# Kernel optimization log

Measured on AMD Instinct MI355X. Metric: run time of the kernel, lower is better.

## Reference

```python
import jax, jax.numpy as jnp
import numpy as np

B, CIN, COUT, K, H, W = 8, 256, 256, 4, 128, 128
BN_EPS = 1e-5


def setup_inputs() -> dict:
    key = jax.random.key(0)
    ks = jax.random.split(key, 12)
    n = lambda i, shape, scale: jax.random.normal(ks[i], shape, jnp.float32) * scale
    return {
        "x": jax.random.normal(ks[0], (B, CIN, H, W), jnp.float32),
        "conv_w": n(1, (COUT, CIN), 0.05),
        "conv_b": n(2, (COUT,), 0.02),
        "off_w": n(3, (K, 2, CIN), 0.02),   # k offset convs, each 1x1 -> 2 channels
        "off_b": n(4, (K, 2), 0.02),
        "wgt_w": n(5, (K, CIN), 0.05),      # weight conv 1x1 -> k channels (softmax over k)
        "wgt_b": n(6, (K,), 0.02),
        "gamma": 1.0 + n(7, (COUT,), 0.1),
        "beta": n(8, (COUT,), 0.1),
        "run_mean": n(9, (COUT,), 0.05),
        "run_var": 1.0 + 0.1 * jax.random.uniform(ks[10], (COUT,), jnp.float32),
        "out_w": n(11, (CIN, COUT), 0.05),
        "out_b": jnp.zeros((CIN,), jnp.float32),
    }


def bilinear_sample(img, gx, gy):
    """F.grid_sample(mode='bilinear', padding_mode='zeros', align_corners=True).
    img: [B,C,H,W]; gx,gy: [B,H,W] normalized coords in [-1,1]."""
    b, c, h, w = img.shape
    x = (gx + 1.0) * 0.5 * (w - 1)  # unnormalize (align_corners=True)
    y = (gy + 1.0) * 0.5 * (h - 1)
    x0 = jnp.floor(x)
    y0 = jnp.floor(y)
    wx1 = x - x0
    wy1 = y - y0
    imgf = img.reshape(b, c, h * w)

    def gather(xi, yi, wgt):
        valid = (xi >= 0) & (xi <= w - 1) & (yi >= 0) & (yi <= h - 1)
        xic = jnp.clip(xi, 0, w - 1).astype(jnp.int32)
        yic = jnp.clip(yi, 0, h - 1).astype(jnp.int32)
        idx = (yic * w + xic).reshape(b, 1, h * w)
        v = jnp.take_along_axis(imgf, idx, axis=2).reshape(b, c, h, w)
        return v * (wgt * valid)[:, None]  # zeros padding: OOB corners contribute 0

    return (gather(x0, y0, (1 - wx1) * (1 - wy1))
            + gather(x0 + 1, y0, wx1 * (1 - wy1))
            + gather(x0, y0 + 1, (1 - wx1) * wy1)
            + gather(x0 + 1, y0 + 1, wx1 * wy1))


def reference(x, conv_w, conv_b, off_w, off_b, wgt_w, wgt_b,
              gamma, beta, run_mean, run_var, out_w, out_b):
    # 1x1 projection conv
    proj = jnp.einsum('bchw,oc->bohw', x, conv_w) + conv_b[:, None, None]
    # k offset branches at once: [K,B,2,H,W]
    flows = jnp.einsum('bchw,koc->kbohw', x, off_w) + off_b[:, None, :, None, None]
    # per-branch softmax weights: [B,K,H,W]
    logits = jnp.einsum('bchw,kc->bkhw', x, wgt_w) + wgt_b[None, :, None, None]
    weights = jax.nn.softmax(logits, axis=1)
    # base grid + flow, normalized to [-1,1]
    grid_x = jnp.arange(W, dtype=jnp.float32)[None, None, None, :]  # broadcast over k,b,h
    grid_y = jnp.arange(H, dtype=jnp.float32)[None, None, :, None]
    vx = grid_x + flows[:, :, 0]  # [K,B,H,W]
    vy = grid_y + flows[:, :, 1]
    gxn = 2.0 * vx / max(W - 1, 1) - 1.0
    gyn = 2.0 * vy / max(H - 1, 1) - 1.0
    feats = jax.vmap(lambda gx, gy: bilinear_sample(proj, gx, gy))(gxn, gyn)  # [K,B,C,H,W]
    # repeat_interleave(weights, out_ch) * cat(feats) then split+sum == weighted sum over k
    fsum = jnp.einsum('kbchw,bkhw->bchw', feats, weights)
    feat = proj + fsum  # dropout in eval mode = identity
    # BatchNorm2d (eval: running stats)
    inv = gamma / jnp.sqrt(run_var + BN_EPS)
    feat = (feat - run_mean[:, None, None]) * inv[:, None, None] + beta[:, None, None]
    return jnp.einsum('bchw,oc->bohw', feat, out_w) + out_b[:, None, None]
```

## Files before the change

kernel.cpp:

```cpp
#include <hip/hip_runtime.h>
#include <cstddef>
#include <cstdint>

#define B_    8
#define CIN_  256
#define COUT_ 256
#define K_    4
#define H_    128
#define W_    128
#define HW_   (H_ * W_)
#define P_    (B_ * HW_)
#define BN_EPS 1e-5f

typedef __attribute__((ext_vector_type(8))) short bf16x8_t;
typedef __attribute__((ext_vector_type(4))) float f32x4_t;

__device__ __forceinline__ unsigned short f2bf(float f) {
    unsigned int u = __float_as_uint(f);
    u += 0x7fffu + ((u >> 16) & 1u);
    return (unsigned short)(u >> 16);
}
__device__ __forceinline__ float2 up2(unsigned int u) {
    return make_float2(__uint_as_float(u << 16), __uint_as_float(u & 0xffff0000u));
}
__device__ __forceinline__ void fma2(float2& d, float s, float2 v) {
    d.x = fmaf(s, v.x, d.x);
    d.y = fmaf(s, v.y, d.y);
}

#define GL2LDS(g, l)                                                                     \
    __builtin_amdgcn_global_load_lds((const __attribute__((address_space(1))) void*)(g), \
                                     (__attribute__((address_space(3))) void*)(l), 16, 0, 0)

__global__ __launch_bounds__(256) void k_prep(
    const float* __restrict__ conv_w, const float* __restrict__ out_w,
    const float* __restrict__ gamma, const float* __restrict__ beta,
    const float* __restrict__ rmean, const float* __restrict__ rvar,
    const float* __restrict__ out_b, const float* __restrict__ off_w,
    const float* __restrict__ wgt_w,
    unsigned short* __restrict__ wA, unsigned short* __restrict__ wB,
    float* __restrict__ bias2, unsigned short* __restrict__ wB2)
{
    const int t = threadIdx.x;
    if (blockIdx.x < 64) {
        const int i = (blockIdx.x * 256 + t) * 4;
        float4 a = *(const float4*)&conv_w[i];
        uint2 pa;
        pa.x = (unsigned)f2bf(a.x) | ((unsigned)f2bf(a.y) << 16);
        pa.y = (unsigned)f2bf(a.z) | ((unsigned)f2bf(a.w) << 16);
        *(uint2*)&wA[i] = pa;
    } else if (blockIdx.x == 64) {
        __shared__ float sinv[256], sd[256];
        const float iv = gamma[t] * rsqrtf(rvar[t] + BN_EPS);
        sinv[t] = iv;
        sd[t]   = beta[t] - rmean[t] * iv;
        __syncthreads();
        float acc = out_b[t];
        for (int c = 0; c < 256; c += 4) {
            const float4 wv = *(const float4*)&out_w[t * 256 + c];
            acc += sd[c] * wv.x + sd[c + 1] * wv.y + sd[c + 2] * wv.z + sd[c + 3] * wv.w;
            uint2 p;
            p.x = (unsigned)f2bf(wv.x * sinv[c])     | ((unsigned)f2bf(wv.y * sinv[c + 1]) << 16);
            p.y = (unsigned)f2bf(wv.z * sinv[c + 2]) | ((unsigned)f2bf(wv.w * sinv[c + 3]) << 16);
            *(uint2*)&wB[t * 256 + c] = p;
        }
        bias2[t] = acc;
    } else {
        for (int j = 0; j < 16; ++j) {
            float v = 0.f;
            if (j < 8)       v = off_w[j * 256 + t];
            else if (j < 12) v = wgt_w[(j - 8) * 256 + t];
            wB2[j * 256 + t] = f2bf(v);
        }
    }
}

__global__ __launch_bounds__(512, 2) void k_fproj(
    const float* __restrict__ x, const unsigned short* __restrict__ wA,
    const unsigned short* __restrict__ wB2, const float* __restrict__ conv_b,
    const float* __restrict__ off_b, const float* __restrict__ wgt_b,
    unsigned short* __restrict__ proj, float4* __restrict__ tabW,
    int4* __restrict__ tabI)
{
    __shared__ alignas(16) char smem[57856];
    char*           AsB  = smem;
    char*           Bs   = smem + 16384;
    float*          fbuf = (float*)(smem + 49152);
    unsigned short* ep   = (unsigned short*)smem;

    const int t   = threadIdx.x;
    const int w   = t >> 6;
    const int l   = t & 63;
    const int lr  = l & 15;
    const int lq  = l >> 4;
    const int wm2 = w & 1;
    const int wn4 = w >> 1;
    const int chg = t & 15;
    const int pxg = t >> 4;
    const int p0  = blockIdx.x * 128;
    const float* xb = x + (size_t)(p0 >> 14) * (256 * HW_) + (p0 & (HW_ - 1)) + pxg * 4;

    f32x4_t acc[4][4];
#pragma unroll
    for (int i = 0; i < 4; ++i)
#pragma unroll
        for (int j = 0; j < 4; ++j) acc[i][j] = (f32x4_t){0.f, 0.f, 0.f, 0.f};
    f32x4_t acc2 = (f32x4_t){0.f, 0.f, 0.f, 0.f};

    float4 f[4], fn[4];
#pragma unroll
    for (int i = 0; i < 4; ++i)
        f[i] = *(const float4*)&xb[(size_t)(chg * 4 + i) * HW_];

    for (int ks = 0; ks < 4; ++ks) {
#pragma unroll
        for (int o = 0; o < 4; ++o) {
            const int px = pxg * 4 + o;
            const float v0 = (o == 0) ? f[0].x : (o == 1) ? f[0].y : (o == 2) ? f[0].z : f[0].w;
            const float v1 = (o == 0) ? f[1].x : (o == 1) ? f[1].y : (o == 2) ? f[1].z : f[1].w;
            const float v2 = (o == 0) ? f[2].x : (o == 1) ? f[2].y : (o == 2) ? f[2].z : f[2].w;
            const float v3 = (o == 0) ? f[3].x : (o == 1) ? f[3].y : (o == 2) ? f[3].z : f[3].w;
            uint2 u;
            u.x = (unsigned)f2bf(v0) | ((unsigned)f2bf(v1) << 16);
            u.y = (unsigned)f2bf(v2) | ((unsigned)f2bf(v3) << 16);
            *(uint2*)(AsB + ((px * 128 + chg * 8) ^ ((px & 7) << 4))) = u;
        }
#pragma unroll
        for (int s = 0; s < 4; ++s) {
            const int idx = w * 4 + s;
            const unsigned short* g = wA + (size_t)((idx & 15) * 16 + lr) * 256
                                      + ks * 64 + (idx >> 4) * 32 + lq * 8;
            GL2LDS(g, Bs + idx * 1024);
        }
        if (ks < 3) {
#pragma unroll
            for (int i = 0; i < 4; ++i)
                fn[i] = *(const float4*)&xb[(size_t)((ks + 1) * 64 + chg * 4 + i) * HW_];
        }
        __syncthreads();
        {
            const int px = w * 16 + lr;
#pragma unroll
            for (int kc = 0; kc < 2; ++kc) {
                const bf16x8_t a2 = *(const bf16x8_t*)(AsB +
                    ((px * 128 + kc * 64 + lq * 16) ^ ((px & 7) << 4)));
                const bf16x8_t b2 = *(const bf16x8_t*)&wB2[lr * 256 + ks * 64 + kc * 32 + lq * 8];
                acc2 = __builtin_amdgcn_mfma_f32_16x16x32_bf16(a2, b2, acc2, 0, 0, 0);
            }
        }
#pragma unroll
        for (int kc = 0; kc < 2; ++kc) {
            bf16x8_t af[4], bfr[4];
#pragma unroll
            for (int i = 0; i < 4; ++i) {
                const int px = (wm2 * 4 + i) * 16 + lr;
                af[i] = *(const bf16x8_t*)(AsB +
                    ((px * 128 + kc * 64 + lq * 16) ^ ((px & 7) << 4)));
            }
#pragma unroll
            for (int j = 0; j < 4; ++j)
                bfr[j] = *(const bf16x8_t*)(Bs + (kc * 16 + wn4 * 4 + j) * 1024 + l * 16);
#pragma unroll
            for (int i = 0; i < 4; ++i)
#pragma unroll
                for (int j = 0; j < 4; ++j)
                    acc[i][j] = __builtin_amdgcn_mfma_f32_16x16x32_bf16(af[i], bfr[j],
                                                                        acc[i][j], 0, 0, 0);
        }
        __syncthreads();
        if (ks < 3) {
#pragma unroll
            for (int i = 0; i < 4; ++i) f[i] = fn[i];
        }
    }

#pragma unroll
    for (int r = 0; r < 4; ++r)
        fbuf[(w * 16 + lq * 4 + r) * 17 + lr] = acc2[r];
    __syncthreads();

    if (t < 128) {
        const int p = p0 + t;
        float a[12];
#pragma unroll
        for (int j = 0; j < 12; ++j) a[j] = fbuf[t * 17 + j];

        const int hw = p & (HW_ - 1);
        const int wx = hw & (W_ - 1);
        const int hy = hw >> 7;
        float lg[4];
#pragma unroll
        for (int k = 0; k < 4; ++k) lg[k] = a[8 + k] + wgt_b[k];
        const float m  = fmaxf(fmaxf(lg[0], lg[1]), fmaxf(lg[2], lg[3]));
        const float e0 = __expf(lg[0] - m), e1 = __expf(lg[1] - m);
        const float e2 = __expf(lg[2] - m), e3 = __expf(lg[3] - m);
        const float sinv = 1.f / (e0 + e1 + e2 + e3);
        const float wk[4] = {e0 * sinv, e1 * sinv, e2 * sinv, e3 * sinv};

#pragma unroll
        for (int k = 0; k < 4; ++k) {
            const float sx = (float)wx + a[k * 2 + 0] + off_b[k * 2 + 0];
            const float sy = (float)hy + a[k * 2 + 1] + off_b[k * 2 + 1];
            const float x0f = floorf(sx), y0f = floorf(sy);
            const float fx = sx - x0f, fy = sy - y0f;
            const float vx0 = (x0f >= 0.f  && x0f <= (float)(W_ - 1)) ? 1.f : 0.f;
            const float vx1 = (x0f >= -1.f && x0f <= (float)(W_ - 2)) ? 1.f : 0.f;
            const float vy0 = (y0f >= 0.f  && y0f <= (float)(H_ - 1)) ? 1.f : 0.f;
            const float vy1 = (y0f >= -1.f && y0f <= (float)(H_ - 2)) ? 1.f : 0.f;
            const int x0 = (int)x0f, y0 = (int)y0f;
            const int cx0 = min(max(x0, 0), W_ - 1);
            const int cx1 = min(max(x0 + 1, 0), W_ - 1);
            const int cy0 = min(max(y0, 0), H_ - 1);
            const int cy1 = min(max(y0 + 1, 0), H_ - 1);
            float4 wv;
            wv.x = (1.f - fx) * (1.f - fy) * wk[k] * vx0 * vy0;
            wv.y = fx * (1.f - fy) * wk[k] * vx1 * vy0;
            wv.z = (1.f - fx) * fy * wk[k] * vx0 * vy1;
            wv.w = fx * fy * wk[k] * vx1 * vy1;
            int4 ov;
            ov.x = (cy0 * W_ + cx0) * 256;
            ov.y = (cy0 * W_ + cx1) * 256;
            ov.z = (cy1 * W_ + cx0) * 256;
            ov.w = (cy1 * W_ + cx1) * 256;
            tabW[(size_t)k * P_ + p] = wv;
            tabI[(size_t)k * P_ + p] = ov;
        }
    }

    for (int h = 0; h < 2; ++h) {
        if ((wn4 >> 1) == h) {
#pragma unroll
            for (int j = 0; j < 4; ++j) {
                const int ncol = wn4 * 64 + j * 16 + lr;
                const float bv = conv_b[ncol];
                const int cl = (wn4 & 1) * 64 + j * 16 + lr;
#pragma unroll
                for (int i = 0; i < 4; ++i)
#pragma unroll
                    for (int r = 0; r < 4; ++r) {
                        const int row = (wm2 * 4 + i) * 16 + lq * 4 + r;
                        ep[row * 132 + cl] = f2bf(acc[i][j][r] + bv);
                    }
            }
        }
        __syncthreads();
#pragma unroll
        for (int pass = 0; pass < 8; ++pass) {
            const int row = pass * 16 + (t >> 5);
            const int c4  = (t & 31) * 4;
            const uint2 v = *(const uint2*)&ep[row * 132 + c4];
            *(uint2*)&proj[(size_t)(p0 + row) * 256 + h * 128 + c4] = v;
        }
        __syncthreads();
    }
}

#define GEMM_STAGE_AND_MFMA(A_, W_ptr_, smem_)                                              \
    char* As = smem_;                                                                       \
    char* Bs = smem_ + 16384;                                                               \
    const int w  = t >> 6;                                                                  \
    const int l  = t & 63;                                                                  \
    const int lr = l & 15;                                                                  \
    const int lq = l >> 4;                                                                  \
    f32x4_t acc[4][4];                                                                      \
    _Pragma("unroll") for (int i = 0; i < 4; ++i)                                           \
        _Pragma("unroll") for (int j = 0; j < 4; ++j)                                       \
            acc[i][j] = (f32x4_t){0.f, 0.f, 0.f, 0.f};                                      \
    const int wm = (w & 1) * 4;                                                             \
    const int wn = (w >> 1) * 4;                                                            \
    _Pragma("unroll") for (int ks = 0; ks < 4; ++ks) {                                      \
        const int k0 = ks * 64;                                                             \
        __syncthreads();                                                                    \
        _Pragma("unroll") for (int i = 0; i < 2; ++i) {                                     \
            const int mt = 2 * w + i;                                                       \
            _Pragma("unroll") for (int kc = 0; kc < 2; ++kc) {                              \
                const unsigned short* g =                                                   \
                    A_ + (size_t)(p0 + mt * 16 + lr) * 256 + k0 + kc * 32 + lq * 8;         \
                GL2LDS(g, As + (kc * 8 + mt) * 1024);                                       \
            }                                                                               \
        }                                                                                   \
        _Pragma("unroll") for (int i = 0; i < 2; ++i) {                                     \
            const int nt = 2 * w + i;                                                       \
            _Pragma("unroll") for (int kc = 0; kc < 2; ++kc) {                              \
                const unsigned short* g =                                                   \
                    W_ptr_ + (size_t)(n0 + nt * 16 + lr) * 256 + k0 + kc * 32 + lq * 8;     \
                GL2LDS(g, Bs + (kc * 8 + nt) * 1024);                                       \
            }                                                                               \
        }                                                                                   \
        __syncthreads();                                                                    \
        _Pragma("unroll") for (int kc = 0; kc < 2; ++kc) {                                  \
            bf16x8_t af[4], bfr[4];                                                         \
            _Pragma("unroll") for (int i = 0; i < 4; ++i)                                   \
                af[i] = *(const bf16x8_t*)(As + (kc * 8 + wm + i) * 1024 + l * 16);         \
            _Pragma("unroll") for (int j = 0; j < 4; ++j)                                   \
                bfr[j] = *(const bf16x8_t*)(Bs + (kc * 8 + wn + j) * 1024 + l * 16);        \
            _Pragma("unroll") for (int i = 0; i < 4; ++i)                                   \
                _Pragma("unroll") for (int j = 0; j < 4; ++j)                               \
                    acc[i][j] =                                                             \
                        __builtin_amdgcn_mfma_f32_16x16x32_bf16(af[i], bfr[j], acc[i][j],   \
                                                                0, 0, 0);                   \
        }                                                                                   \
    }

__global__ __launch_bounds__(256, 3) void k_out(
    const unsigned short* __restrict__ A, const unsigned short* __restrict__ Wb,
    const float* __restrict__ bias, float* __restrict__ Cout)
{
    __shared__ alignas(16) char smem[32768];
    const int t  = threadIdx.x;
    const int bx = blockIdx.x;
    const int n0 = (bx & 1) * 128;
    const int p0 = (bx >> 1) * 128;

    GEMM_STAGE_AND_MFMA(A, Wb, smem)

    const int mh = (w & 1) * 64, nh = (w >> 1) * 64;
    const int b   = p0 >> 14;
    const int hw0 = p0 & (HW_ - 1);
#pragma unroll
    for (int j = 0; j < 4; ++j) {
        const int   n  = n0 + nh + j * 16 + lr;
        const float bb = bias[n];
#pragma unroll
        for (int i = 0; i < 4; ++i) {
            f32x4_t v = acc[i][j];
            v[0] += bb; v[1] += bb; v[2] += bb; v[3] += bb;
            *(f32x4_t*)&Cout[(size_t)(b * 256 + n) * HW_ + hw0 + mh + i * 16 + lq * 4] = v;
        }
    }
}

__global__ __launch_bounds__(256) void k_sample(
    const unsigned short* __restrict__ proj, const float4* __restrict__ tabW,
    const int4* __restrict__ tabI, unsigned short* __restrict__ feat)
{
    const int t  = threadIdx.x;
    const int w  = t >> 6;
    const int l  = t & 63;
    const int ph = l >> 5;
    const int c0 = (l & 31) * 8;

    const int pbase = blockIdx.x * 16;
    const int b = pbase >> 14;
    const unsigned short* projb = proj + (size_t)b * HW_ * 256;

#pragma unroll
    for (int it = 0; it < 2; ++it) {
        const int p = pbase + it * 8 + w * 2 + ph;
        const uint4 rv = *(const uint4*)&proj[(size_t)p * 256 + c0];
        float2 a0 = up2(rv.x), a1 = up2(rv.y), a2 = up2(rv.z), a3 = up2(rv.w);
#pragma unroll
        for (int k = 0; k < 4; ++k) {
            const float4 wv = tabW[(size_t)k * P_ + p];
            const int4   ov = tabI[(size_t)k * P_ + p];
            const uint4 g0 = *(const uint4*)&projb[ov.x + c0];
            const uint4 g1 = *(const uint4*)&projb[ov.y + c0];
            const uint4 g2 = *(const uint4*)&projb[ov.z + c0];
            const uint4 g3 = *(const uint4*)&projb[ov.w + c0];
            fma2(a0, wv.x, up2(g0.x)); fma2(a1, wv.x, up2(g0.y));
            fma2(a2, wv.x, up2(g0.z)); fma2(a3, wv.x, up2(g0.w));
            fma2(a0, wv.y, up2(g1.x)); fma2(a1, wv.y, up2(g1.y));
            fma2(a2, wv.y, up2(g1.z)); fma2(a3, wv.y, up2(g1.w));
            fma2(a0, wv.z, up2(g2.x)); fma2(a1, wv.z, up2(g2.y));
            fma2(a2, wv.z, up2(g2.z)); fma2(a3, wv.z, up2(g2.w));
            fma2(a0, wv.w, up2(g3.x)); fma2(a1, wv.w, up2(g3.y));
            fma2(a2, wv.w, up2(g3.z)); fma2(a3, wv.w, up2(g3.w));
        }
        uint4 o;
        o.x = (unsigned)f2bf(a0.x) | ((unsigned)f2bf(a0.y) << 16);
        o.y = (unsigned)f2bf(a1.x) | ((unsigned)f2bf(a1.y) << 16);
        o.z = (unsigned)f2bf(a2.x) | ((unsigned)f2bf(a2.y) << 16);
        o.w = (unsigned)f2bf(a3.x) | ((unsigned)f2bf(a3.y) << 16);
        *(uint4*)&feat[(size_t)p * 256 + c0] = o;
    }
}

extern "C" void kernel_launch(void* const* d_in, const int* in_sizes, int n_in,
                              void* d_out, int out_size, void* d_ws, size_t ws_size,
                              hipStream_t stream)
{
    const float* x      = (const float*)d_in[0];
    const float* conv_w = (const float*)d_in[1];
    const float* conv_b = (const float*)d_in[2];
    const float* off_w  = (const float*)d_in[3];
    const float* off_b  = (const float*)d_in[4];
    const float* wgt_w  = (const float*)d_in[5];
    const float* wgt_b  = (const float*)d_in[6];
    const float* gamma  = (const float*)d_in[7];
    const float* beta   = (const float*)d_in[8];
    const float* rmean  = (const float*)d_in[9];
    const float* rvar   = (const float*)d_in[10];
    const float* out_w  = (const float*)d_in[11];
    const float* out_b  = (const float*)d_in[12];

    char* ws = (char*)d_ws;
    unsigned short* wB2  = (unsigned short*)(ws);
    unsigned short* proj = (unsigned short*)(ws + (size_t)67108864);
    unsigned short* feat = (unsigned short*)(ws + (size_t)134217728);
    float4*         tabW = (float4*)(ws + (size_t)201326592);
    int4*           tabI = (int4*)(ws + (size_t)209715200);
    unsigned short* wA   = (unsigned short*)(ws + (size_t)218103808);
    unsigned short* wB   = (unsigned short*)(ws + (size_t)218234880);
    float*          bias2= (float*)(ws + (size_t)218365952);

    k_prep  <<<66,         256, 0, stream>>>(conv_w, out_w, gamma, beta, rmean, rvar,
                                             out_b, off_w, wgt_w, wA, wB, bias2, wB2);
    k_fproj <<<P_ / 128,   512, 0, stream>>>(x, wA, wB2, conv_b, off_b, wgt_b,
                                             proj, tabW, tabI);
    k_sample<<<P_ / 16,    256, 0, stream>>>(proj, tabW, tabI, feat);
    k_out   <<<(P_/128)*2, 256, 0, stream>>>(feat, wB, bias2, (float*)d_out);
}
```

Before: 392.5 us.

## Fuse bilinear sampling into the output GEMM kernel, dropping feat buffer

```diff
diff --git a/kernel.cpp b/kernel.cpp
--- a/kernel.cpp
+++ b/kernel.cpp
@@ -255,123 +255,113 @@
     }
 }
 
-#define GEMM_STAGE_AND_MFMA(A_, W_ptr_, smem_)                                              \
-    char* As = smem_;                                                                       \
-    char* Bs = smem_ + 16384;                                                               \
-    const int w  = t >> 6;                                                                  \
-    const int l  = t & 63;                                                                  \
-    const int lr = l & 15;                                                                  \
-    const int lq = l >> 4;                                                                  \
-    f32x4_t acc[4][4];                                                                      \
-    _Pragma("unroll") for (int i = 0; i < 4; ++i)                                           \
-        _Pragma("unroll") for (int j = 0; j < 4; ++j)                                       \
-            acc[i][j] = (f32x4_t){0.f, 0.f, 0.f, 0.f};                                      \
-    const int wm = (w & 1) * 4;                                                             \
-    const int wn = (w >> 1) * 4;                                                            \
-    _Pragma("unroll") for (int ks = 0; ks < 4; ++ks) {                                      \
-        const int k0 = ks * 64;                                                             \
-        __syncthreads();                                                                    \
-        _Pragma("unroll") for (int i = 0; i < 2; ++i) {                                     \
-            const int mt = 2 * w + i;                                                       \
-            _Pragma("unroll") for (int kc = 0; kc < 2; ++kc) {                              \
-                const unsigned short* g =                                                   \
-                    A_ + (size_t)(p0 + mt * 16 + lr) * 256 + k0 + kc * 32 + lq * 8;         \
-                GL2LDS(g, As + (kc * 8 + mt) * 1024);                                       \
-            }                                                                               \
-        }                                                                                   \
-        _Pragma("unroll") for (int i = 0; i < 2; ++i) {                                     \
-            const int nt = 2 * w + i;                                                       \
-            _Pragma("unroll") for (int kc = 0; kc < 2; ++kc) {                              \
-                const unsigned short* g =                                                   \
-                    W_ptr_ + (size_t)(n0 + nt * 16 + lr) * 256 + k0 + kc * 32 + lq * 8;     \
-                GL2LDS(g, Bs + (kc * 8 + nt) * 1024);                                       \
-            }                                                                               \
-        }                                                                                   \
-        __syncthreads();                                                                    \
-        _Pragma("unroll") for (int kc = 0; kc < 2; ++kc) {                                  \
-            bf16x8_t af[4], bfr[4];                                                         \
-            _Pragma("unroll") for (int i = 0; i < 4; ++i)                                   \
-                af[i] = *(const bf16x8_t*)(As + (kc * 8 + wm + i) * 1024 + l * 16);         \
-            _Pragma("unroll") for (int j = 0; j < 4; ++j)                                   \
-                bfr[j] = *(const bf16x8_t*)(Bs + (kc * 8 + wn + j) * 1024 + l * 16);        \
-            _Pragma("unroll") for (int i = 0; i < 4; ++i)                                   \
-                _Pragma("unroll") for (int j = 0; j < 4; ++j)                               \
-                    acc[i][j] =                                                             \
-                        __builtin_amdgcn_mfma_f32_16x16x32_bf16(af[i], bfr[j], acc[i][j],   \
-                                                                0, 0, 0);                   \
-        }                                                                                   \
-    }
-
-__global__ __launch_bounds__(256, 3) void k_out(
-    const unsigned short* __restrict__ A, const unsigned short* __restrict__ Wb,
-    const float* __restrict__ bias, float* __restrict__ Cout)
+__global__ __launch_bounds__(512, 2) void k_fout(
+    const unsigned short* __restrict__ proj, const unsigned short* __restrict__ wB,
+    const float* __restrict__ bias2, const float4* __restrict__ tabW,
+    const int4* __restrict__ tabI, float* __restrict__ Cout)
 {
-    __shared__ alignas(16) char smem[32768];
-    const int t  = threadIdx.x;
-    const int bx = blockIdx.x;
-    const int n0 = (bx & 1) * 128;
-    const int p0 = (bx >> 1) * 128;
-
-    GEMM_STAGE_AND_MFMA(A, Wb, smem)
-
-    const int mh = (w & 1) * 64, nh = (w >> 1) * 64;
-    const int b   = p0 >> 14;
-    const int hw0 = p0 & (HW_ - 1);
+    __shared__ alignas(16) char smem[65536];
+    char* featA = smem;
+    char* Bs    = smem + 16384;
+    char* sWl   = smem + 49152;
+    char* sIl   = smem + 57344;
+
+    const int t   = threadIdx.x;
+    const int w   = t >> 6;
+    const int l   = t & 63;
+    const int lr  = l & 15;
+    const int lq  = l >> 4;
+    const int wm2 = w & 1;
+    const int wn4 = w >> 1;
+    const int px0 = blockIdx.x * 128;
+    const int b   = px0 >> 14;
+    const int hw0 = px0 & (HW_ - 1);
+    const unsigned short* projb = proj + (size_t)b * HW_ * 256;
+
+    GL2LDS(&tabW[(size_t)(w >> 1) * P_ + px0 + (w & 1) * 64 + l], sWl + w * 1024);
+    GL2LDS(&tabI[(size_t)(w >> 1) * P_ + px0 + (w & 1) * 64 + l], sIl + w * 1024);
+
+    f32x4_t acc[4][4];
+#pragma unroll
+    for (int i = 0; i < 4; ++i)
+#pragma unroll
+        for (int j = 0; j < 4; ++j) acc[i][j] = (f32x4_t){0.f, 0.f, 0.f, 0.f};
+
+    __syncthreads();
+
+    for (int ks = 0; ks < 4; ++ks) {
+#pragma unroll
+        for (int s = 0; s < 4; ++s) {
+            const int idx = w * 4 + s;
+            const unsigned short* g = wB + (size_t)((idx & 15) * 16 + lr) * 256
+                                      + ks * 64 + (idx >> 4) * 32 + lq * 8;
+            GL2LDS(g, Bs + idx * 1024);
+        }
+#pragma unroll
+        for (int slot = 0; slot < 2; ++slot) {
+            const int s  = t + slot * 512;
+            const int px = s >> 3;
+            const int cs = (s & 7) * 8;
+            const int ch = ks * 64 + cs;
+            const uint4 rv = *(const uint4*)&proj[(size_t)(px0 + px) * 256 + ch];
+            float2 a0 = up2(rv.x), a1 = up2(rv.y), a2 = up2(rv.z), a3 = up2(rv.w);
+#pragma unroll
+            for (int k = 0; k < 4; ++k) {
+                const float4 wv = *(const float4*)(sWl + k * 2048 + px * 16);
+                const int4   ov = *(const int4*)(sIl + k * 2048 + px * 16);
+                const uint4 g0 = *(const uint4*)&projb[ov.x + ch];
+                const uint4 g1 = *(const uint4*)&projb[ov.y + ch];
+                const uint4 g2 = *(const uint4*)&projb[ov.z + ch];
+                const uint4 g3 = *(const uint4*)&projb[ov.w + ch];
+                fma2(a0, wv.x, up2(g0.x)); fma2(a1, wv.x, up2(g0.y));
+                fma2(a2, wv.x, up2(g0.z)); fma2(a3, wv.x, up2(g0.w));
+                fma2(a0, wv.y, up2(g1.x)); fma2(a1, wv.y, up2(g1.y));
+                fma2(a2, wv.y, up2(g1.z)); fma2(a3, wv.y, up2(g1.w));
+                fma2(a0, wv.z, up2(g2.x)); fma2(a1, wv.z, up2(g2.y));
+                fma2(a2, wv.z, up2(g2.z)); fma2(a3, wv.z, up2(g2.w));
+                fma2(a0, wv.w, up2(g3.x)); fma2(a1, wv.w, up2(g3.y));
+                fma2(a2, wv.w, up2(g3.z)); fma2(a3, wv.w, up2(g3.w));
+            }
+            uint4 o;
+            o.x = (unsigned)f2bf(a0.x) | ((unsigned)f2bf(a0.y) << 16);
+            o.y = (unsigned)f2bf(a1.x) | ((unsigned)f2bf(a1.y) << 16);
+            o.z = (unsigned)f2bf(a2.x) | ((unsigned)f2bf(a2.y) << 16);
+            o.w = (unsigned)f2bf(a3.x) | ((unsigned)f2bf(a3.y) << 16);
+            *(uint4*)(featA + ((px * 128 + cs * 2) ^ ((px & 7) << 4))) = o;
+        }
+        __syncthreads();
+#pragma unroll
+        for (int kc = 0; kc < 2; ++kc) {
+            bf16x8_t af[4], bfr[4];
+#pragma unroll
+            for (int i = 0; i < 4; ++i) {
+                const int px = (wm2 * 4 + i) * 16 + lr;
+                af[i] = *(const bf16x8_t*)(featA +
+                    ((px * 128 + kc * 64 + lq * 16) ^ ((px & 7) << 4)));
+            }
+#pragma unroll
+            for (int j = 0; j < 4; ++j)
+                bfr[j] = *(const bf16x8_t*)(Bs + (kc * 16 + wn4 * 4 + j) * 1024 + l * 16);
+#pragma unroll
+            for (int i = 0; i < 4; ++i)
+#pragma unroll
+                for (int j = 0; j < 4; ++j)
+                    acc[i][j] = __builtin_amdgcn_mfma_f32_16x16x32_bf16(af[i], bfr[j],
+                                                                        acc[i][j], 0, 0, 0);
+        }
+        __syncthreads();
+    }
+
 #pragma unroll
     for (int j = 0; j < 4; ++j) {
-        const int   n  = n0 + nh + j * 16 + lr;
-        const float bb = bias[n];
+        const int   n  = wn4 * 64 + j * 16 + lr;
+        const float bb = bias2[n];
 #pragma unroll
         for (int i = 0; i < 4; ++i) {
             f32x4_t v = acc[i][j];
             v[0] += bb; v[1] += bb; v[2] += bb; v[3] += bb;
-            *(f32x4_t*)&Cout[(size_t)(b * 256 + n) * HW_ + hw0 + mh + i * 16 + lq * 4] = v;
-        }
-    }
-}
-
-__global__ __launch_bounds__(256) void k_sample(
-    const unsigned short* __restrict__ proj, const float4* __restrict__ tabW,
-    const int4* __restrict__ tabI, unsigned short* __restrict__ feat)
-{
-    const int t  = threadIdx.x;
-    const int w  = t >> 6;
-    const int l  = t & 63;
-    const int ph = l >> 5;
-    const int c0 = (l & 31) * 8;
-
-    const int pbase = blockIdx.x * 16;
-    const int b = pbase >> 14;
-    const unsigned short* projb = proj + (size_t)b * HW_ * 256;
-
-#pragma unroll
-    for (int it = 0; it < 2; ++it) {
-        const int p = pbase + it * 8 + w * 2 + ph;
-        const uint4 rv = *(const uint4*)&proj[(size_t)p * 256 + c0];
-        float2 a0 = up2(rv.x), a1 = up2(rv.y), a2 = up2(rv.z), a3 = up2(rv.w);
-#pragma unroll
-        for (int k = 0; k < 4; ++k) {
-            const float4 wv = tabW[(size_t)k * P_ + p];
-            const int4   ov = tabI[(size_t)k * P_ + p];
-            const uint4 g0 = *(const uint4*)&projb[ov.x + c0];
-            const uint4 g1 = *(const uint4*)&projb[ov.y + c0];
-            const uint4 g2 = *(const uint4*)&projb[ov.z + c0];
-            const uint4 g3 = *(const uint4*)&projb[ov.w + c0];
-            fma2(a0, wv.x, up2(g0.x)); fma2(a1, wv.x, up2(g0.y));
-            fma2(a2, wv.x, up2(g0.z)); fma2(a3, wv.x, up2(g0.w));
-            fma2(a0, wv.y, up2(g1.x)); fma2(a1, wv.y, up2(g1.y));
-            fma2(a2, wv.y, up2(g1.z)); fma2(a3, wv.y, up2(g1.w));
-            fma2(a0, wv.z, up2(g2.x)); fma2(a1, wv.z, up2(g2.y));
-            fma2(a2, wv.z, up2(g2.z)); fma2(a3, wv.z, up2(g2.w));
-            fma2(a0, wv.w, up2(g3.x)); fma2(a1, wv.w, up2(g3.y));
-            fma2(a2, wv.w, up2(g3.z)); fma2(a3, wv.w, up2(g3.w));
-        }
-        uint4 o;
-        o.x = (unsigned)f2bf(a0.x) | ((unsigned)f2bf(a0.y) << 16);
-        o.y = (unsigned)f2bf(a1.x) | ((unsigned)f2bf(a1.y) << 16);
-        o.z = (unsigned)f2bf(a2.x) | ((unsigned)f2bf(a2.y) << 16);
-        o.w = (unsigned)f2bf(a3.x) | ((unsigned)f2bf(a3.y) << 16);
-        *(uint4*)&feat[(size_t)p * 256 + c0] = o;
+            *(f32x4_t*)&Cout[(size_t)(b * 256 + n) * HW_ + hw0 + wm2 * 64 + i * 16 + lq * 4] = v;
+        }
     }
 }
 
@@ -396,17 +386,15 @@
     char* ws = (char*)d_ws;
     unsigned short* wB2  = (unsigned short*)(ws);
     unsigned short* proj = (unsigned short*)(ws + (size_t)67108864);
-    unsigned short* feat = (unsigned short*)(ws + (size_t)134217728);
     float4*         tabW = (float4*)(ws + (size_t)201326592);
     int4*           tabI = (int4*)(ws + (size_t)209715200);
     unsigned short* wA   = (unsigned short*)(ws + (size_t)218103808);
     unsigned short* wB   = (unsigned short*)(ws + (size_t)218234880);
     float*          bias2= (float*)(ws + (size_t)218365952);
 
-    k_prep  <<<66,         256, 0, stream>>>(conv_w, out_w, gamma, beta, rmean, rvar,
-                                             out_b, off_w, wgt_w, wA, wB, bias2, wB2);
-    k_fproj <<<P_ / 128,   512, 0, stream>>>(x, wA, wB2, conv_b, off_b, wgt_b,
-                                             proj, tabW, tabI);
-    k_sample<<<P_ / 16,    256, 0, stream>>>(proj, tabW, tabI, feat);
-    k_out   <<<(P_/128)*2, 256, 0, stream>>>(feat, wB, bias2, (float*)d_out);
-}
+    k_prep  <<<66,       256, 0, stream>>>(conv_w, out_w, gamma, beta, rmean, rvar,
+                                           out_b, off_w, wgt_w, wA, wB, bias2, wB2);
+    k_fproj <<<P_ / 128, 512, 0, stream>>>(x, wA, wB2, conv_b, off_b, wgt_b,
+                                           proj, tabW, tabI);
+    k_fout  <<<P_ / 128, 512, 0, stream>>>(proj, wB, bias2, tabW, tabI, (float*)d_out);
+}
```

Measured after the change: 418.7 us. +6.7%, slower.
